# Performance work log

Hardware: AMD Instinct MI355X
Metric: run time of the kernel (lower is better)

The kernel has to match this reference:

```python
import jax, jax.numpy as jnp
import numpy as np

B, T, NE, NH, HD = 4, 1024, 768, 12, 64
CURV = 0.0
EPS = 1e-6
LN_EPS = 1e-5
ROPE_BASE = 10000.0


def project(x, k):
    # Lift Euclidean vector onto Lorentz hyperboloid with curvature K = exp(k):
    # time coord t = sqrt(K + ||x||^2) so that <lx, lx>_L = -K.
    K = jnp.exp(k)
    t = jnp.sqrt(K + jnp.sum(x * x, axis=-1, keepdims=True))
    return jnp.concatenate([t, x], axis=-1)


def lorentz_distance(lq, lk, k):
    # lq, lk: (B, H, T, D+1); k: (1, H, 1, 1) log-curvature.
    # d = sqrt(K) * arccosh(clamp(-<q,k>_L / K, 1+eps))
    K = jnp.exp(k)
    inner = (jnp.einsum('bhid,bhjd->bhij', lq[..., 1:], lk[..., 1:])
             - jnp.einsum('bhi,bhj->bhij', lq[..., 0], lk[..., 0]))
    c = jnp.clip(-inner / K, 1.0 + EPS, None)
    return jnp.sqrt(K) * jnp.arccosh(c)


def lorentz_norm(x):
    # sqrt(|<x,x>_L|) with <x,x>_L = -x0^2 + ||xs||^2  (keepdim)
    inner = -x[..., 0:1] ** 2 + jnp.sum(x[..., 1:] ** 2, axis=-1, keepdims=True)
    return jnp.sqrt(jnp.clip(-inner, EPS, None))


def rotary_tables():
    inv_freq = 1.0 / (ROPE_BASE ** (np.arange(0, HD, 2, dtype=np.float32) / HD))
    t = np.arange(T, dtype=np.float32)
    freqs = np.outer(t, inv_freq)  # (T, HD/2)
    cos = jnp.asarray(np.cos(freqs))[None, :, None, :]  # (1,T,1,HD/2)
    sin = jnp.asarray(np.sin(freqs))[None, :, None, :]
    return cos, sin


def apply_rotary(x, cos, sin):
    # x: (B, T, H, HD)
    x1, x2 = x[..., : HD // 2], x[..., HD // 2:]
    return jnp.concatenate([x1 * cos + x2 * sin, -x1 * sin + x2 * cos], axis=-1)


def layernorm(y, g, b):
    m = jnp.mean(y, axis=-1, keepdims=True)
    v = jnp.mean((y - m) ** 2, axis=-1, keepdims=True)
    return (y - m) / jnp.sqrt(v + LN_EPS) * g + b


def setup_inputs() -> dict:
    key = jax.random.key(0)
    ks = jax.random.split(key, 8)
    s = 0.02
    return {
        'x': jax.random.normal(ks[0], (B, T, NE), dtype=jnp.float32),
        'block_curvature': jnp.asarray(CURV, dtype=jnp.float32),
        'mlp_curvature': jnp.asarray(CURV, dtype=jnp.float32),
        'attn_curvatures': jnp.ones((1, NH, 1, 1), dtype=jnp.float32) * CURV,
        'qkv_w': jax.random.normal(ks[1], (3 * NE, NE + 1), dtype=jnp.float32) * s,
        'attn_proj_w': jax.random.normal(ks[2], (NE, (HD + 1) * NH), dtype=jnp.float32) * s,
        'attn_proj_b': jnp.zeros((NE,), dtype=jnp.float32),
        'mlp_expand_w': jax.random.normal(ks[3], (4 * NE + 3, NE + 1), dtype=jnp.float32) * s,
        'mlp_expand_b': jnp.zeros((4 * NE + 3,), dtype=jnp.float32),
        'mlp_shrink_w': jax.random.normal(ks[4], (NE, 4 * (NE + 1)), dtype=jnp.float32) * s,
        'mlp_shrink_b': jnp.zeros((NE,), dtype=jnp.float32),
        'ln_g': jnp.ones((NE,), dtype=jnp.float32),
        'ln_b': jnp.zeros((NE,), dtype=jnp.float32),
    }


def reference(x, block_curvature, mlp_curvature, attn_curvatures, qkv_w,
              attn_proj_w, attn_proj_b, mlp_expand_w, mlp_expand_b,
              mlp_shrink_w, mlp_shrink_b, ln_g, ln_b):
    cos, sin = rotary_tables()
    causal_bias = jnp.where(
        jnp.triu(jnp.ones((T, T), dtype=bool), k=1), -jnp.inf, 0.0).astype(jnp.float32)

    def block_norm(lx):
        return project(layernorm(lx[..., 1:], ln_g, ln_b), block_curvature)

    def attn(lx):
        qkv = lx @ qkv_w.T  # (B, T, 3*NE)
        q, k, v = jnp.split(qkv, 3, axis=-1)
        q = apply_rotary(q.reshape(B, T, NH, HD), cos, sin)
        k = apply_rotary(k.reshape(B, T, NH, HD), cos, sin)
        v = v.reshape(B, T, NH, HD)
        lq = project(q.transpose(0, 2, 1, 3), attn_curvatures)  # (B,H,T,HD+1)
        lk = project(k.transpose(0, 2, 1, 3), attn_curvatures)
        lv = project(v.transpose(0, 2, 1, 3), attn_curvatures)
        dis = lorentz_distance(lq, lk, attn_curvatures)  # (B,H,T,T)
        aw = jax.nn.softmax(-dis + causal_bias, axis=-1)
        a = jnp.einsum('bhij,bhjd->bhid', aw, lv)  # (B,H,T,HD+1)
        a = a * jnp.sqrt(jnp.exp(attn_curvatures)) / lorentz_norm(a)
        a = a.transpose(0, 2, 1, 3).reshape(B, T, NH * (HD + 1))
        a = a @ attn_proj_w.T + attn_proj_b
        return project(a, block_curvature)

    def mlp(lx):
        h = lx @ mlp_expand_w.T + mlp_expand_b  # (B,T,4*NE+3)
        h = project(h, mlp_curvature)[..., 1:]  # drop time coord back to 4*NE+3
        h = jax.nn.gelu(h, approximate=False)
        h = project(h, mlp_curvature)  # (B,T,4*(NE+1))
        h = h @ mlp_shrink_w.T + mlp_shrink_b
        return project(h, block_curvature)

    def skip(lx, f_lx):
        return project(lx[..., 1:] + f_lx[..., 1:], block_curvature)

    lx = project(x, block_curvature)  # (B,T,NE+1)
    lx = skip(lx, attn(block_norm(lx)))
    lx = skip(lx, mlp(block_norm(lx)))
    return lx
```

## Files before the change

kernel.cpp:

```cpp
#include <hip/hip_runtime.h>
#include <cmath>

typedef unsigned short ushort_t;
typedef __attribute__((ext_vector_type(8))) short short8;
typedef __attribute__((ext_vector_type(4))) float floatx4;

#define NH    12
#define T     1024
#define ROWS  4096
#define NE    768
#define KPA   832
#define KPB   3136
#define NEXP  3200
#define HEXP  3075
#define NSPLIT 3

__device__ __forceinline__ ushort_t f2bf(float f) {
  union { float f; unsigned u; } v; v.f = f;
  unsigned r = v.u + 0x7fffu + ((v.u >> 16) & 1u);
  return (ushort_t)(r >> 16);
}
__device__ __forceinline__ ushort_t f2bf_trunc(float f) {
  union { float f; unsigned u; } v; v.f = f;
  return (ushort_t)(v.u >> 16);
}
__device__ __forceinline__ float bf2f(ushort_t b) {
  union { unsigned u; float f; } v; v.u = ((unsigned)b) << 16;
  return v.f;
}
__device__ __forceinline__ float blk_reduce_sum(float v, float* sm) {
  #pragma unroll
  for (int o = 32; o > 0; o >>= 1) v += __shfl_xor(v, o, 64);
  int lane = threadIdx.x & 63, w = threadIdx.x >> 6;
  __syncthreads();
  if (lane == 0) sm[w] = v;
  __syncthreads();
  return sm[0] + sm[1] + sm[2] + sm[3];
}
__device__ __forceinline__ float red16_sum(float v) {
  #pragma unroll
  for (int o = 1; o < 16; o <<= 1) v += __shfl_xor(v, o, 64);
  return v;
}

#define NB_A 7488
#define NB_B 2496
#define NB_C 10400
#define NB_D 9408
#define NB_E 16
__device__ __forceinline__ void cvt_elem(ushort_t* __restrict__ dst,
                                         const float* __restrict__ src,
                                         int idx, int srcRows, int srcK, int dstK) {
  int r = idx / dstK, c = idx - r * dstK;
  dst[idx] = (r < srcRows && c < srcK) ? f2bf(src[(size_t)r * srcK + c]) : (ushort_t)0;
}
__global__ __launch_bounds__(256) void prep_kernel(
    ushort_t* __restrict__ qkv_wb, const float* __restrict__ qkvw,
    ushort_t* __restrict__ proj_wb, const float* __restrict__ projw,
    ushort_t* __restrict__ exp_wb, const float* __restrict__ expw,
    ushort_t* __restrict__ shr_wb, const float* __restrict__ shrw,
    ushort_t* __restrict__ aout_bf,
    const float* __restrict__ xin, const float* __restrict__ g,
    const float* __restrict__ bb, const float* __restrict__ curv,
    ushort_t* __restrict__ lnp) {
  __shared__ float sm[4];
  int blk = blockIdx.x;
  int tid = threadIdx.x;
  if (blk < NB_A) {
    cvt_elem(qkv_wb, qkvw, blk * 256 + tid, 2304, 769, KPA);
  } else if (blk < NB_A + NB_B) {
    cvt_elem(proj_wb, projw, (blk - NB_A) * 256 + tid, 768, 780, KPA);
  } else if (blk < NB_A + NB_B + NB_C) {
    cvt_elem(exp_wb, expw, (blk - NB_A - NB_B) * 256 + tid, HEXP, 769, KPA);
  } else if (blk < NB_A + NB_B + NB_C + NB_D) {
    cvt_elem(shr_wb, shrw, (blk - NB_A - NB_B - NB_C) * 256 + tid, 768, 3076, KPB);
  } else if (blk < NB_A + NB_B + NB_C + NB_D + NB_E) {
    int r = (blk - NB_A - NB_B - NB_C - NB_D) * 256 + tid;
    ushort_t* p = aout_bf + (size_t)r * KPA + 780;
    #pragma unroll
    for (int j = 0; j < KPA - 780; ++j) p[j] = 0;
  } else {
    const int row = blk - (NB_A + NB_B + NB_C + NB_D + NB_E);
    const float* xr = xin + (size_t)row * NE;
    float xv[3];
    float s = 0.f, ss = 0.f;
    #pragma unroll
    for (int i = 0; i < 3; ++i) {
      xv[i] = xr[tid + 256 * i];
      s += xv[i]; ss += xv[i] * xv[i];
    }
    s = blk_reduce_sum(s, sm);
    ss = blk_reduce_sum(ss, sm);
    float mean = s * (1.f / 768.f);
    float var = ss * (1.f / 768.f) - mean * mean;
    float rstd = rsqrtf(var + 1e-5f);
    float yv[3]; float ys = 0.f;
    #pragma unroll
    for (int i = 0; i < 3; ++i) {
      int c = tid + 256 * i;
      yv[i] = (xv[i] - mean) * rstd * g[c] + bb[c];
      ys += yv[i] * yv[i];
    }
    ys = blk_reduce_sum(ys, sm);
    float tc = sqrtf(expf(curv[0]) + ys);
    ushort_t* orow = lnp + (size_t)row * KPA;
    #pragma unroll
    for (int i = 0; i < 3; ++i) orow[1 + tid + 256 * i] = f2bf(yv[i]);
    if (tid == 0) orow[0] = f2bf(tc);
    if (tid < KPA - 769) orow[769 + tid] = 0;
  }
}

__global__ __launch_bounds__(256) void gemm_bf16(
    const ushort_t* __restrict__ A, int lda,
    const ushort_t* __restrict__ W, int ldw,
    void* __restrict__ Cout, int ldc,
    int nkTot, int cpt,
    const float* __restrict__ bias, int biasN,
    const float* __restrict__ res, int ldres,
    int outMode, void* __restrict__ Cp) {
  __shared__ ushort_t As[128 * 64];
  __shared__ ushort_t Bs[128 * 64];
  const int tid = threadIdx.x;
  const int w = tid >> 6, lane = tid & 63;
  const int rowBase = (int)blockIdx.y << 7;
  const int colBase = (int)blockIdx.x << 7;
  const int wm = (w & 1) * 64, wn = (w >> 1) * 64;
  const int lm = lane & 15, quad = lane >> 4;
  const int p0 = quad ^ (lm & 7);

  floatx4 acc[4][4];
  #pragma unroll
  for (int i = 0; i < 4; ++i)
    #pragma unroll
    for (int j = 0; j < 4; ++j) {
      floatx4 z = {0.f, 0.f, 0.f, 0.f};
      acc[i][j] = z;
    }

  const int kt0 = (int)blockIdx.z * cpt;
  const int kt1 = min(nkTot, kt0 + cpt);
  for (int kt = kt0; kt < kt1; ++kt) {
    __syncthreads();
    #pragma unroll
    for (int j = 0; j < 4; ++j) {
      int ci = j * 256 + tid;
      int r = ci >> 3;
      int g = (ci & 7) ^ (r & 7);
      const ushort_t* ga = A + (size_t)(rowBase + r) * lda + kt * 64 + g * 8;
      const ushort_t* gb = W + (size_t)(colBase + r) * ldw + kt * 64 + g * 8;
      __builtin_amdgcn_global_load_lds(
          (const __attribute__((address_space(1))) void*)ga,
          (__attribute__((address_space(3))) void*)&As[(j * 256 + w * 64) * 8],
          16, 0, 0);
      __builtin_amdgcn_global_load_lds(
          (const __attribute__((address_space(1))) void*)gb,
          (__attribute__((address_space(3))) void*)&Bs[(j * 256 + w * 64) * 8],
          16, 0, 0);
    }
    __syncthreads();

    #pragma unroll
    for (int s = 0; s < 2; ++s) {
      const int ps = s ? (p0 ^ 4) : p0;
      short8 af[4], bfr[4];
      #pragma unroll
      for (int i = 0; i < 4; ++i) {
        af[i]  = *(const short8*)&As[(wm + i * 16 + lm) * 64 + ps * 8];
        bfr[i] = *(const short8*)&Bs[(wn + i * 16 + lm) * 64 + ps * 8];
      }
      #pragma unroll
      for (int i = 0; i < 4; ++i)
        #pragma unroll
        for (int jn = 0; jn < 4; ++jn)
          acc[i][jn] = __builtin_amdgcn_mfma_f32_16x16x32_bf16(
              af[i], bfr[jn], acc[i][jn], 0, 0, 0);
    }
  }

  if (gridDim.z > 1) {
    ushort_t* dst = (ushort_t*)Cp + (size_t)blockIdx.z * ROWS * ldc;
    #pragma unroll
    for (int i = 0; i < 4; ++i)
      #pragma unroll
      for (int jn = 0; jn < 4; ++jn) {
        const int col = colBase + wn + jn * 16 + lm;
        #pragma unroll
        for (int rg = 0; rg < 4; ++rg) {
          const int row = rowBase + wm + i * 16 + quad * 4 + rg;
          dst[(size_t)row * ldc + col] = f2bf(acc[i][jn][rg]);
        }
      }
  } else if (outMode == 1) {
    ushort_t* C = (ushort_t*)Cout;
    #pragma unroll
    for (int i = 0; i < 4; ++i)
      #pragma unroll
      for (int jn = 0; jn < 4; ++jn) {
        const int col = colBase + wn + jn * 16 + lm;
        const float bv = bias ? ((col < biasN) ? bias[col] : 0.f) : 0.f;
        #pragma unroll
        for (int rg = 0; rg < 4; ++rg) {
          const int row = rowBase + wm + i * 16 + quad * 4 + rg;
          C[(size_t)row * ldc + col] = f2bf(acc[i][jn][rg] + bv);
        }
      }
  } else {
    float* C = (float*)Cout;
    #pragma unroll
    for (int i = 0; i < 4; ++i)
      #pragma unroll
      for (int jn = 0; jn < 4; ++jn) {
        const int col = colBase + wn + jn * 16 + lm;
        const float bv = bias ? ((col < biasN) ? bias[col] : 0.f) : 0.f;
        #pragma unroll
        for (int rg = 0; rg < 4; ++rg) {
          const int row = rowBase + wm + i * 16 + quad * 4 + rg;
          float o = acc[i][jn][rg] + bv;
          if (res) o += res[(size_t)row * ldres + col];
          C[(size_t)row * ldc + col] = o;
        }
      }
  }
}

__global__ __launch_bounds__(256) void rope_project(
    const ushort_t* __restrict__ qkv, const float* __restrict__ ac,
    ushort_t* __restrict__ qb, ushort_t* __restrict__ kb, ushort_t* __restrict__ vtb,
    float* __restrict__ q0, float* __restrict__ k0, float* __restrict__ v0) {
  int gid = blockIdx.x * 4 + (threadIdx.x >> 6);
  int lane = threadIdx.x & 63;
  int h = gid % NH;
  int bt = gid / NH;
  int t = bt & (T - 1);
  int b = bt >> 10;
  size_t base = (size_t)bt * 2304 + h * 64;
  float qv = bf2f(qkv[base + lane]);
  float kv = bf2f(qkv[base + 768 + lane]);
  float vv = bf2f(qkv[base + 1536 + lane]);
  int f = lane & 31;
  float ang = (float)t * powf(10000.f, -(float)f * (1.f / 32.f));
  float sn, cs;
  sincosf(ang, &sn, &cs);
  float qp = __shfl(qv, lane ^ 32, 64);
  float kp = __shfl(kv, lane ^ 32, 64);
  float qr = (lane < 32) ? (qv * cs + qp * sn) : (-qp * sn + qv * cs);
  float kr = (lane < 32) ? (kv * cs + kp * sn) : (-kp * sn + kv * cs);
  float Kh = expf(ac[h]);
  float sq = qr * qr, sk = kr * kr, sv = vv * vv;
  #pragma unroll
  for (int o = 32; o > 0; o >>= 1) {
    sq += __shfl_xor(sq, o, 64);
    sk += __shfl_xor(sk, o, 64);
    sv += __shfl_xor(sv, o, 64);
  }
  size_t idx = ((size_t)(b * NH + h) * T + t);
  qb[idx * 64 + lane] = f2bf(qr);
  kb[idx * 64 + lane] = f2bf(kr);
  vtb[(size_t)(b * NH + h) * (64 * T) + (size_t)lane * T + t] = f2bf(vv);
  if (lane == 0) {
    q0[idx] = sqrtf(Kh + sq);
    k0[idx] = sqrtf(Kh + sk);
    v0[idx] = sqrtf(Kh + sv);
  }
}

__global__ __launch_bounds__(256) void attn_kernel(
    const ushort_t* __restrict__ qb, const ushort_t* __restrict__ kb,
    const ushort_t* __restrict__ vtb,
    const float* __restrict__ q0, const float* __restrict__ k0,
    const float* __restrict__ v0,
    const float* __restrict__ ac,
    ushort_t* __restrict__ Opart, float* __restrict__ lpart,
    float* __restrict__ a0part) {
  __shared__ ushort_t Qs[64 * 64];
  __shared__ ushort_t Ks[64 * 64];
  __shared__ ushort_t Vts[64 * 64];
  __shared__ ushort_t Ps[64 * 72];

  const int sIdx = blockIdx.x;
  const int qtile = (int)gridDim.y - 1 - (int)blockIdx.y;
  const int bh = blockIdx.z;
  const int h = bh % NH;
  const int qt0 = qtile * 64;
  const int tid = threadIdx.x;
  const int w = tid >> 6, lane = tid & 63;
  const int lm = lane & 15, quad = lane >> 4;
  const int wm = w * 16;
  const int sw = lm & 7;

  const int n = qtile + 1;
  const int kbeg = (n * sIdx) / NSPLIT;
  const int kend = (n * (sIdx + 1)) / NSPLIT;
  const size_t pb = (size_t)(sIdx * 48 + bh) * T;

  if (kbeg >= kend) {
    #pragma unroll
    for (int r = 0; r < 4; ++r) {
      const int i = qt0 + wm + quad * 4 + r;
      ushort_t* orow = Opart + (pb + i) * 64;
      #pragma unroll
      for (int nt = 0; nt < 4; ++nt) orow[nt * 16 + lm] = 0;
      if (lm == 0) { lpart[pb + i] = 0.f; a0part[pb + i] = 0.f; }
    }
    return;
  }

  const float Kh = expf(ac[h]);
  const float sqrtK = sqrtf(Kh);
  const float invK = 1.0f / Kh;
  const float nsK = -sqrtK;
  const bool k1 = (Kh == 1.0f);

  {
    const ushort_t* qt = qb + ((size_t)bh * T + qt0) * 64;
    #pragma unroll
    for (int j = 0; j < 2; ++j) {
      int e = (j * 4 + w) * 512 + lane * 8;
      int r = e >> 6, chs = (e >> 3) & 7;
      int clog = (chs ^ (r & 7)) * 8;
      __builtin_amdgcn_global_load_lds(
          (const __attribute__((address_space(1))) void*)(qt + r * 64 + clog),
          (__attribute__((address_space(3))) void*)&Qs[(j * 4 + w) * 512],
          16, 0, 0);
    }
  }
  __syncthreads();
  short8 qf0 = *(const short8*)&Qs[(wm + lm) * 64 + ((0 + quad) ^ sw) * 8];
  short8 qf1 = *(const short8*)&Qs[(wm + lm) * 64 + ((4 + quad) ^ sw) * 8];
  float q0rv[4];
  #pragma unroll
  for (int r = 0; r < 4; ++r)
    q0rv[r] = q0[(size_t)bh * T + qt0 + wm + quad * 4 + r];

  float lsum[4], a0r[4];
  floatx4 oacc[4];
  #pragma unroll
  for (int r = 0; r < 4; ++r) { lsum[r] = 0.f; a0r[r] = 0.f; }
  #pragma unroll
  for (int nt = 0; nt < 4; ++nt) { floatx4 z = {0.f,0.f,0.f,0.f}; oacc[nt] = z; }

  for (int kt = kbeg; kt < kend; ++kt) {
    const int j0 = kt * 64;
    __syncthreads();
    {
      const ushort_t* ktile = kb + ((size_t)bh * T + j0) * 64;
      const ushort_t* vbh = vtb + (size_t)bh * (64 * T);
      #pragma unroll
      for (int j = 0; j < 2; ++j) {
        int e = (j * 4 + w) * 512 + lane * 8;
        int r = e >> 6, chs = (e >> 3) & 7;
        int clog = (chs ^ (r & 7)) * 8;
        __builtin_amdgcn_global_load_lds(
            (const __attribute__((address_space(1))) void*)(ktile + r * 64 + clog),
            (__attribute__((address_space(3))) void*)&Ks[(j * 4 + w) * 512],
            16, 0, 0);
        __builtin_amdgcn_global_load_lds(
            (const __attribute__((address_space(1))) void*)(vbh + (size_t)r * T + j0 + clog),
            (__attribute__((address_space(3))) void*)&Vts[(j * 4 + w) * 512],
            16, 0, 0);
      }
    }
    float k0i[4], v0v[4];
    #pragma unroll
    for (int jt = 0; jt < 4; ++jt) {
      k0i[jt] = k0[(size_t)bh * T + j0 + jt * 16 + lm] * invK;
      v0v[jt] = v0[(size_t)bh * T + j0 + jt * 16 + lm];
    }
    __syncthreads();

    floatx4 sacc[4];
    #pragma unroll
    for (int jt = 0; jt < 4; ++jt) {
      const int krow = jt * 16 + lm;
      short8 kf0 = *(const short8*)&Ks[krow * 64 + ((0 + quad) ^ sw) * 8];
      short8 kf1 = *(const short8*)&Ks[krow * 64 + ((4 + quad) ^ sw) * 8];
      floatx4 z = {0.f, 0.f, 0.f, 0.f};
      z = __builtin_amdgcn_mfma_f32_16x16x32_bf16(qf0, kf0, z, 0, 0, 0);
      z = __builtin_amdgcn_mfma_f32_16x16x32_bf16(qf1, kf1, z, 0, 0, 0);
      sacc[jt] = z;
    }

    const bool diag = (kt == qtile);
    if (k1) {
      #pragma unroll
      for (int r = 0; r < 4; ++r) {
        const int i = qt0 + wm + quad * 4 + r;
        float ls = 0.f, a0s = 0.f;
        #pragma unroll
        for (int jt = 0; jt < 4; ++jt) {
          float c = fmaf(-invK, sacc[jt][r], q0rv[r] * k0i[jt]);
          c = fmaxf(c, 1.000001f);
          float p = c - sqrtf(fmaf(c, c, -1.f));
          if (diag && (j0 + jt * 16 + lm > i)) p = 0.f;
          ushort_t pb2 = f2bf_trunc(p);
          Ps[(wm + quad * 4 + r) * 72 + jt * 16 + lm] = pb2;
          float pf = bf2f(pb2);
          ls += pf;
          a0s = fmaf(pf, v0v[jt], a0s);
        }
        lsum[r] += ls;
        a0r[r] += a0s;
      }
    } else {
      #pragma unroll
      for (int r = 0; r < 4; ++r) {
        const int i = qt0 + wm + quad * 4 + r;
        float ls = 0.f, a0s = 0.f;
        #pragma unroll
        for (int jt = 0; jt < 4; ++jt) {
          float c = fmaf(-invK, sacc[jt][r], q0rv[r] * k0i[jt]);
          c = fmaxf(c, 1.000001f);
          float z = c + sqrtf(fmaf(c, c, -1.f));
          float p = __builtin_amdgcn_exp2f(nsK * __builtin_amdgcn_logf(z));
          if (diag && (j0 + jt * 16 + lm > i)) p = 0.f;
          ushort_t pb2 = f2bf_trunc(p);
          Ps[(wm + quad * 4 + r) * 72 + jt * 16 + lm] = pb2;
          float pf = bf2f(pb2);
          ls += pf;
          a0s = fmaf(pf, v0v[jt], a0s);
        }
        lsum[r] += ls;
        a0r[r] += a0s;
      }
    }

    short8 pf0 = *(const short8*)&Ps[(wm + lm) * 72 + quad * 8];
    short8 pf1 = *(const short8*)&Ps[(wm + lm) * 72 + 32 + quad * 8];
    #pragma unroll
    for (int nt = 0; nt < 4; ++nt) {
      const int vrow = nt * 16 + lm;
      short8 vf0 = *(const short8*)&Vts[vrow * 64 + ((0 + quad) ^ sw) * 8];
      short8 vf1 = *(const short8*)&Vts[vrow * 64 + ((4 + quad) ^ sw) * 8];
      oacc[nt] = __builtin_amdgcn_mfma_f32_16x16x32_bf16(pf0, vf0, oacc[nt], 0, 0, 0);
      oacc[nt] = __builtin_amdgcn_mfma_f32_16x16x32_bf16(pf1, vf1, oacc[nt], 0, 0, 0);
    }
  }

  #pragma unroll
  for (int r = 0; r < 4; ++r) {
    float lf = red16_sum(lsum[r]);
    float a0f = red16_sum(a0r[r]);
    const int i = qt0 + wm + quad * 4 + r;
    ushort_t* orow = Opart + (pb + i) * 64;
    #pragma unroll
    for (int nt = 0; nt < 4; ++nt) orow[nt * 16 + lm] = f2bf(oacc[nt][r]);
    if (lm == 0) { lpart[pb + i] = lf; a0part[pb + i] = a0f; }
  }
}

__global__ __launch_bounds__(256) void attn_combine(
    const ushort_t* __restrict__ Opart, const float* __restrict__ lpart,
    const float* __restrict__ a0part,
    const float* __restrict__ ac, ushort_t* __restrict__ aout) {
  const int widx = blockIdx.x * 4 + (threadIdx.x >> 6);
  const int lane = threadIdx.x & 63;
  const int bh = widx >> 10;
  const int t = widx & 1023;
  const int h = bh % NH, b = bh / NH;
  float L = 0.f, A0 = 0.f, O = 0.f;
  #pragma unroll
  for (int sp = 0; sp < NSPLIT; ++sp) {
    const size_t r = (size_t)(sp * 48 + bh) * T + t;
    L += lpart[r];
    A0 += a0part[r];
    O += bf2f(Opart[r * 64 + lane]);
  }
  const float invl = 1.f / L;
  float av = O * invl;
  float ssq = av * av;
  #pragma unroll
  for (int o = 32; o > 0; o >>= 1) ssq += __shfl_xor(ssq, o, 64);
  float a0n = A0 * invl;
  float nsq = fmaxf(a0n * a0n - ssq, 1e-6f);
  float Kh = expf(ac[h]);
  float scale = sqrtf(Kh) * rsqrtf(nsq);
  ushort_t* orow = aout + (size_t)(b * T + t) * KPA + h * 65;
  orow[1 + lane] = f2bf(av * scale);
  if (lane == 0) orow[0] = f2bf(a0n * scale);
}

__global__ __launch_bounds__(256) void gelu_project(
    const ushort_t* __restrict__ hsrc, const float* __restrict__ curv,
    ushort_t* __restrict__ hp) {
  __shared__ float sm[4];
  const int row = blockIdx.x;
  const int tid = threadIdx.x;
  const ushort_t* hr = hsrc + (size_t)row * NEXP;
  float gv[13];
  float ss = 0.f;
  #pragma unroll
  for (int i = 0; i < 13; ++i) {
    int c = tid + 256 * i;
    float xx = (c < HEXP) ? bf2f(hr[c]) : 0.f;
    float gg = 0.5f * xx * (1.f + erff(xx * 0.70710678118654752f));
    gv[i] = gg; ss += gg * gg;
  }
  ss = blk_reduce_sum(ss, sm);
  float tc = sqrtf(expf(curv[0]) + ss);
  ushort_t* orow = hp + (size_t)row * KPB;
  #pragma unroll
  for (int i = 0; i < 13; ++i) {
    int c = tid + 256 * i;
    if (c < HEXP) orow[1 + c] = f2bf(gv[i]);
  }
  if (tid == 0) orow[0] = f2bf(tc);
  if (tid < KPB - (HEXP + 1)) orow[HEXP + 1 + tid] = 0;
}

__global__ __launch_bounds__(256) void reduce_ln_project(
    const ushort_t* __restrict__ Cp, int nsplit,
    const float* __restrict__ bias, const float* __restrict__ res,
    float* __restrict__ x2out,
    const float* __restrict__ g, const float* __restrict__ bb,
    const float* __restrict__ curv, ushort_t* __restrict__ lnp) {
  __shared__ float sm[4];
  const int row = blockIdx.x;
  const int tid = threadIdx.x;
  float xv[3];
  float s = 0.f, ss = 0.f;
  #pragma unroll
  for (int i = 0; i < 3; ++i) {
    const int c = tid + 256 * i;
    float v = bias[c] + res[(size_t)row * NE + c];
    for (int sp = 0; sp < nsplit; ++sp)
      v += bf2f(Cp[(size_t)sp * ROWS * NE + (size_t)row * NE + c]);
    x2out[(size_t)row * NE + c] = v;
    xv[i] = v;
    s += v; ss += v * v;
  }
  s = blk_reduce_sum(s, sm);
  ss = blk_reduce_sum(ss, sm);
  float mean = s * (1.f / 768.f);
  float var = ss * (1.f / 768.f) - mean * mean;
  float rstd = rsqrtf(var + 1e-5f);
  float yv[3]; float ys = 0.f;
  #pragma unroll
  for (int i = 0; i < 3; ++i) {
    int c = tid + 256 * i;
    yv[i] = (xv[i] - mean) * rstd * g[c] + bb[c];
    ys += yv[i] * yv[i];
  }
  ys = blk_reduce_sum(ys, sm);
  float tc = sqrtf(expf(curv[0]) + ys);
  ushort_t* orow = lnp + (size_t)row * KPA;
  #pragma unroll
  for (int i = 0; i < 3; ++i) orow[1 + tid + 256 * i] = f2bf(yv[i]);
  if (tid == 0) orow[0] = f2bf(tc);
  if (tid < KPA - 769) orow[769 + tid] = 0;
}

__global__ __launch_bounds__(256) void reduce_final_project(
    const ushort_t* __restrict__ Cp, int nsplit,
    const float* __restrict__ bias, const float* __restrict__ res,
    const float* __restrict__ curv, float* __restrict__ out) {
  __shared__ float sm[4];
  const int row = blockIdx.x;
  const int tid = threadIdx.x;
  float v[3]; float ss = 0.f;
  #pragma unroll
  for (int i = 0; i < 3; ++i) {
    const int c = tid + 256 * i;
    float t = bias[c] + res[(size_t)row * NE + c];
    for (int sp = 0; sp < nsplit; ++sp)
      t += bf2f(Cp[(size_t)sp * ROWS * NE + (size_t)row * NE + c]);
    v[i] = t; ss += t * t;
  }
  ss = blk_reduce_sum(ss, sm);
  float tc = sqrtf(expf(curv[0]) + ss);
  float* o = out + (size_t)row * 769;
  #pragma unroll
  for (int i = 0; i < 3; ++i) o[1 + tid + 256 * i] = v[i];
  if (tid == 0) o[0] = tc;
}

extern "C" void kernel_launch(void* const* d_in, const int* in_sizes, int n_in,
                              void* d_out, int out_size, void* d_ws, size_t ws_size,
                              hipStream_t stream) {
  (void)in_sizes; (void)n_in; (void)out_size; (void)ws_size;
  const float* x     = (const float*)d_in[0];
  const float* bc    = (const float*)d_in[1];
  const float* mc    = (const float*)d_in[2];
  const float* ac    = (const float*)d_in[3];
  const float* qkvw  = (const float*)d_in[4];
  const float* projw = (const float*)d_in[5];
  const float* projb = (const float*)d_in[6];
  const float* expw  = (const float*)d_in[7];
  const float* expb  = (const float*)d_in[8];
  const float* shrw  = (const float*)d_in[9];
  const float* shrb  = (const float*)d_in[10];
  const float* lng   = (const float*)d_in[11];
  const float* lnb   = (const float*)d_in[12];
  float* out = (float*)d_out;

  float* x2 = (float*)d_ws;
  ushort_t* qkv_wb  = (ushort_t*)(x2 + (size_t)ROWS * NE);
  ushort_t* proj_wb = qkv_wb + (size_t)2304 * KPA;
  ushort_t* exp_wb  = proj_wb + (size_t)768 * KPA;
  ushort_t* shr_wb  = exp_wb + (size_t)NEXP * KPA;
  ushort_t* lnp_bf  = shr_wb + (size_t)768 * KPB;
  ushort_t* aout_bf = lnp_bf + (size_t)ROWS * KPA;
  char* r2 = (char*)(aout_bf + (size_t)ROWS * KPA);
  ushort_t* qkvb = (ushort_t*)r2;
  ushort_t* qbb = qkvb + (size_t)ROWS * 2304;
  ushort_t* kbb = qbb + (size_t)48 * T * 64;
  ushort_t* vtb = kbb + (size_t)48 * T * 64;
  float* q0b = (float*)(vtb + (size_t)48 * T * 64);
  float* k0b = q0b + (size_t)48 * T;
  float* v0b = k0b + (size_t)48 * T;
  ushort_t* Opart = (ushort_t*)(v0b + (size_t)48 * T);
  float* lpart = (float*)(Opart + (size_t)NSPLIT * 48 * T * 64);
  float* a0part = lpart + (size_t)NSPLIT * 48 * T;
  ushort_t* ppartP = (ushort_t*)r2;
  ushort_t* hbbf = (ushort_t*)r2;
  ushort_t* hp_bf = hbbf + (size_t)ROWS * NEXP;
  ushort_t* ppartS = hp_bf + (size_t)ROWS * KPB;

  prep_kernel<<<NB_A + NB_B + NB_C + NB_D + NB_E + ROWS, 256, 0, stream>>>(
      qkv_wb, qkvw, proj_wb, projw, exp_wb, expw, shr_wb, shrw, aout_bf,
      x, lng, lnb, bc, lnp_bf);
  gemm_bf16<<<dim3(2304 / 128, ROWS / 128, 1), 256, 0, stream>>>(
      lnp_bf, KPA, qkv_wb, KPA, qkvb, 2304, KPA / 64, KPA / 64,
      nullptr, 0, nullptr, 0, 1, nullptr);
  rope_project<<<(ROWS * NH) / 4, 256, 0, stream>>>(qkvb, ac, qbb, kbb, vtb, q0b, k0b, v0b);
  attn_kernel<<<dim3(NSPLIT, T / 64, 48), 256, 0, stream>>>(
      qbb, kbb, vtb, q0b, k0b, v0b, ac, Opart, lpart, a0part);
  attn_combine<<<(48 * T) / 4, 256, 0, stream>>>(Opart, lpart, a0part, ac, aout_bf);
  gemm_bf16<<<dim3(768 / 128, ROWS / 128, 2), 256, 0, stream>>>(
      aout_bf, KPA, proj_wb, KPA, nullptr, NE, KPA / 64, 7,
      nullptr, 0, nullptr, 0, 0, ppartP);
  reduce_ln_project<<<ROWS, 256, 0, stream>>>(
      ppartP, 2, projb, x, x2, lng, lnb, bc, lnp_bf);
  gemm_bf16<<<dim3(NEXP / 128, ROWS / 128, 1), 256, 0, stream>>>(
      lnp_bf, KPA, exp_wb, KPA, hbbf, NEXP, KPA / 64, KPA / 64,
      expb, HEXP, nullptr, 0, 1, nullptr);
  gelu_project<<<ROWS, 256, 0, stream>>>(hbbf, mc, hp_bf);
  gemm_bf16<<<dim3(768 / 128, ROWS / 128, 4), 256, 0, stream>>>(
      hp_bf, KPB, shr_wb, KPB, nullptr, NE, KPB / 64, 13,
      nullptr, 0, nullptr, 0, 0, ppartS);
  reduce_final_project<<<ROWS, 256, 0, stream>>>(
      ppartS, 4, shrb, x2, bc, out);
}
```

Measured before the change: 376.2 us.

## Double-buffer GEMM and attention tile loads; widen attention query tile to 128

The bf16 GEMM now double-buffers its A and B shared-memory tiles. It issues the next k-tile's global-to-LDS loads before running the MFMAs on the current tile, which cuts the per-iteration barrier count to one. The attention kernel moves to 512-thread blocks covering 128 query rows, with double-buffered K/V tiles and the k0/v0 row scalars prefetched one tile ahead. Rope's powf is replaced with a hardware exp2 using a precomputed log2 constant. In exchange, LDS use per block is higher and the attention grid has fewer, larger blocks, which may lower occupancy and worsen load balance across the causal split.

```diff
diff --git a/kernel.cpp b/kernel.cpp
--- a/kernel.cpp
+++ b/kernel.cpp
@@ -119,8 +119,8 @@
     const float* __restrict__ bias, int biasN,
     const float* __restrict__ res, int ldres,
     int outMode, void* __restrict__ Cp) {
-  __shared__ ushort_t As[128 * 64];
-  __shared__ ushort_t Bs[128 * 64];
+  __shared__ ushort_t As[2][128 * 64];
+  __shared__ ushort_t Bs[2][128 * 64];
   const int tid = threadIdx.x;
   const int w = tid >> 6, lane = tid & 63;
   const int rowBase = (int)blockIdx.y << 7;
@@ -140,8 +140,8 @@
 
   const int kt0 = (int)blockIdx.z * cpt;
   const int kt1 = min(nkTot, kt0 + cpt);
-  for (int kt = kt0; kt < kt1; ++kt) {
-    __syncthreads();
+
+  auto stage = [&](int kt, int bsel) {
     #pragma unroll
     for (int j = 0; j < 4; ++j) {
       int ci = j * 256 + tid;
@@ -151,14 +151,24 @@
       const ushort_t* gb = W + (size_t)(colBase + r) * ldw + kt * 64 + g * 8;
       __builtin_amdgcn_global_load_lds(
           (const __attribute__((address_space(1))) void*)ga,
-          (__attribute__((address_space(3))) void*)&As[(j * 256 + w * 64) * 8],
+          (__attribute__((address_space(3))) void*)&As[bsel][(j * 256 + w * 64) * 8],
           16, 0, 0);
       __builtin_amdgcn_global_load_lds(
           (const __attribute__((address_space(1))) void*)gb,
-          (__attribute__((address_space(3))) void*)&Bs[(j * 256 + w * 64) * 8],
+          (__attribute__((address_space(3))) void*)&Bs[bsel][(j * 256 + w * 64) * 8],
           16, 0, 0);
     }
-    __syncthreads();
+  };
+
+  stage(kt0, 0);
+  asm volatile("s_waitcnt vmcnt(0)" ::: "memory");
+  __builtin_amdgcn_s_barrier();
+  __builtin_amdgcn_sched_barrier(0);
+
+  int cur = 0;
+  for (int kt = kt0; kt < kt1; ++kt) {
+    const bool hasNext = (kt + 1 < kt1);
+    if (hasNext) stage(kt + 1, cur ^ 1);
 
     #pragma unroll
     for (int s = 0; s < 2; ++s) {
@@ -166,8 +176,8 @@
       short8 af[4], bfr[4];
       #pragma unroll
       for (int i = 0; i < 4; ++i) {
-        af[i]  = *(const short8*)&As[(wm + i * 16 + lm) * 64 + ps * 8];
-        bfr[i] = *(const short8*)&Bs[(wn + i * 16 + lm) * 64 + ps * 8];
+        af[i]  = *(const short8*)&As[cur][(wm + i * 16 + lm) * 64 + ps * 8];
+        bfr[i] = *(const short8*)&Bs[cur][(wn + i * 16 + lm) * 64 + ps * 8];
       }
       #pragma unroll
       for (int i = 0; i < 4; ++i)
@@ -176,6 +186,13 @@
           acc[i][jn] = __builtin_amdgcn_mfma_f32_16x16x32_bf16(
               af[i], bfr[jn], acc[i][jn], 0, 0, 0);
     }
+
+    if (hasNext) {
+      asm volatile("s_waitcnt vmcnt(0)" ::: "memory");
+      __builtin_amdgcn_s_barrier();
+      __builtin_amdgcn_sched_barrier(0);
+    }
+    cur ^= 1;
   }
 
   if (gridDim.z > 1) {
@@ -239,7 +256,7 @@
   float kv = bf2f(qkv[base + 768 + lane]);
   float vv = bf2f(qkv[base + 1536 + lane]);
   int f = lane & 31;
-  float ang = (float)t * powf(10000.f, -(float)f * (1.f / 32.f));
+  float ang = (float)t * __builtin_amdgcn_exp2f(-(float)f * 0.4152410118661534f);
   float sn, cs;
   sincosf(ang, &sn, &cs);
   float qp = __shfl(qv, lane ^ 32, 64);
@@ -265,7 +282,7 @@
   }
 }
 
-__global__ __launch_bounds__(256) void attn_kernel(
+__global__ __launch_bounds__(512, 4) void attn_kernel(
     const ushort_t* __restrict__ qb, const ushort_t* __restrict__ kb,
     const ushort_t* __restrict__ vtb,
     const float* __restrict__ q0, const float* __restrict__ k0,
@@ -273,23 +290,23 @@
     const float* __restrict__ ac,
     ushort_t* __restrict__ Opart, float* __restrict__ lpart,
     float* __restrict__ a0part) {
-  __shared__ ushort_t Qs[64 * 64];
-  __shared__ ushort_t Ks[64 * 64];
-  __shared__ ushort_t Vts[64 * 64];
-  __shared__ ushort_t Ps[64 * 72];
+  __shared__ ushort_t Qs[128 * 64];
+  __shared__ ushort_t Ks[2][64 * 64];
+  __shared__ ushort_t Vts[2][64 * 64];
+  __shared__ ushort_t Ps[128 * 72];
 
   const int sIdx = blockIdx.x;
   const int qtile = (int)gridDim.y - 1 - (int)blockIdx.y;
   const int bh = blockIdx.z;
   const int h = bh % NH;
-  const int qt0 = qtile * 64;
+  const int qt0 = qtile * 128;
   const int tid = threadIdx.x;
   const int w = tid >> 6, lane = tid & 63;
   const int lm = lane & 15, quad = lane >> 4;
   const int wm = w * 16;
   const int sw = lm & 7;
 
-  const int n = qtile + 1;
+  const int n = 2 * qtile + 2;
   const int kbeg = (n * sIdx) / NSPLIT;
   const int kend = (n * (sIdx + 1)) / NSPLIT;
   const size_t pb = (size_t)(sIdx * 48 + bh) * T;
@@ -313,26 +330,51 @@
   const bool k1 = (Kh == 1.0f);
 
   {
-    const ushort_t* qt = qb + ((size_t)bh * T + qt0) * 64;
+    const ushort_t* qtp = qb + ((size_t)bh * T + qt0) * 64;
     #pragma unroll
     for (int j = 0; j < 2; ++j) {
-      int e = (j * 4 + w) * 512 + lane * 8;
-      int r = e >> 6, chs = (e >> 3) & 7;
-      int clog = (chs ^ (r & 7)) * 8;
+      int ci = j * 512 + tid;
+      int r = ci >> 3;
+      int clog = ((ci & 7) ^ (r & 7)) * 8;
       __builtin_amdgcn_global_load_lds(
-          (const __attribute__((address_space(1))) void*)(qt + r * 64 + clog),
-          (__attribute__((address_space(3))) void*)&Qs[(j * 4 + w) * 512],
+          (const __attribute__((address_space(1))) void*)(qtp + r * 64 + clog),
+          (__attribute__((address_space(3))) void*)&Qs[(j * 8 + w) * 512],
           16, 0, 0);
     }
   }
-  __syncthreads();
-  short8 qf0 = *(const short8*)&Qs[(wm + lm) * 64 + ((0 + quad) ^ sw) * 8];
-  short8 qf1 = *(const short8*)&Qs[(wm + lm) * 64 + ((4 + quad) ^ sw) * 8];
+  const ushort_t* kbase = kb + (size_t)bh * T * 64;
+  const ushort_t* vbh = vtb + (size_t)bh * (64 * T);
+  const float* k0row = k0 + (size_t)bh * T;
+  const float* v0row = v0 + (size_t)bh * T;
+  const int ldr = tid >> 3;
+  const int ldcs = ((tid & 7) ^ (ldr & 7)) * 8;
+  {
+    const int j0 = kbeg * 64;
+    __builtin_amdgcn_global_load_lds(
+        (const __attribute__((address_space(1))) void*)(kbase + (size_t)(j0 + ldr) * 64 + ldcs),
+        (__attribute__((address_space(3))) void*)&Ks[0][w * 512], 16, 0, 0);
+    __builtin_amdgcn_global_load_lds(
+        (const __attribute__((address_space(1))) void*)(vbh + (size_t)ldr * T + j0 + ldcs),
+        (__attribute__((address_space(3))) void*)&Vts[0][w * 512], 16, 0, 0);
+  }
+  float k0n[4], v0n[4];
+  #pragma unroll
+  for (int jt = 0; jt < 4; ++jt) {
+    k0n[jt] = k0row[kbeg * 64 + jt * 16 + lm];
+    v0n[jt] = v0row[kbeg * 64 + jt * 16 + lm];
+  }
   float q0rv[4];
   #pragma unroll
   for (int r = 0; r < 4; ++r)
     q0rv[r] = q0[(size_t)bh * T + qt0 + wm + quad * 4 + r];
 
+  asm volatile("s_waitcnt vmcnt(0)" ::: "memory");
+  __builtin_amdgcn_s_barrier();
+  __builtin_amdgcn_sched_barrier(0);
+
+  const short8 qf0 = *(const short8*)&Qs[(wm + lm) * 64 + ((0 + quad) ^ sw) * 8];
+  const short8 qf1 = *(const short8*)&Qs[(wm + lm) * 64 + ((4 + quad) ^ sw) * 8];
+
   float lsum[4], a0r[4];
   floatx4 oacc[4];
   #pragma unroll
@@ -340,48 +382,45 @@
   #pragma unroll
   for (int nt = 0; nt < 4; ++nt) { floatx4 z = {0.f,0.f,0.f,0.f}; oacc[nt] = z; }
 
+  int cur = 0;
   for (int kt = kbeg; kt < kend; ++kt) {
+    const bool hasNext = (kt + 1 < kend);
+    float k0i[4], v0v[4];
+    #pragma unroll
+    for (int jt = 0; jt < 4; ++jt) { k0i[jt] = k0n[jt] * invK; v0v[jt] = v0n[jt]; }
+
+    if (hasNext) {
+      const int j0n = (kt + 1) * 64;
+      __builtin_amdgcn_global_load_lds(
+          (const __attribute__((address_space(1))) void*)(kbase + (size_t)(j0n + ldr) * 64 + ldcs),
+          (__attribute__((address_space(3))) void*)&Ks[cur ^ 1][w * 512], 16, 0, 0);
+      __builtin_amdgcn_global_load_lds(
+          (const __attribute__((address_space(1))) void*)(vbh + (size_t)ldr * T + j0n + ldcs),
+          (__attribute__((address_space(3))) void*)&Vts[cur ^ 1][w * 512], 16, 0, 0);
+      #pragma unroll
+      for (int jt = 0; jt < 4; ++jt) {
+        k0n[jt] = k0row[j0n + jt * 16 + lm];
+        v0n[jt] = v0row[j0n + jt * 16 + lm];
+      }
+    }
+
     const int j0 = kt * 64;
-    __syncthreads();
-    {
-      const ushort_t* ktile = kb + ((size_t)bh * T + j0) * 64;
-      const ushort_t* vbh = vtb + (size_t)bh * (64 * T);
-      #pragma unroll
-      for (int j = 0; j < 2; ++j) {
-        int e = (j * 4 + w) * 512 + lane * 8;
-        int r = e >> 6, chs = (e >> 3) & 7;
-        int clog = (chs ^ (r & 7)) * 8;
-        __builtin_amdgcn_global_load_lds(
-            (const __attribute__((address_space(1))) void*)(ktile + r * 64 + clog),
-            (__attribute__((address_space(3))) void*)&Ks[(j * 4 + w) * 512],
-            16, 0, 0);
-        __builtin_amdgcn_global_load_lds(
-            (const __attribute__((address_space(1))) void*)(vbh + (size_t)r * T + j0 + clog),
-            (__attribute__((address_space(3))) void*)&Vts[(j * 4 + w) * 512],
-            16, 0, 0);
-      }
-    }
-    float k0i[4], v0v[4];
-    #pragma unroll
-    for (int jt = 0; jt < 4; ++jt) {
-      k0i[jt] = k0[(size_t)bh * T + j0 + jt * 16 + lm] * invK;
-      v0v[jt] = v0[(size_t)bh * T + j0 + jt * 16 + lm];
-    }
-    __syncthreads();
+    const ushort_t* Kc = Ks[cur];
+    const ushort_t* Vc = Vts[cur];
 
     floatx4 sacc[4];
     #pragma unroll
     for (int jt = 0; jt < 4; ++jt) {
       const int krow = jt * 16 + lm;
-      short8 kf0 = *(const short8*)&Ks[krow * 64 + ((0 + quad) ^ sw) * 8];
-      short8 kf1 = *(const short8*)&Ks[krow * 64 + ((4 + quad) ^ sw) * 8];
+      short8 kf0 = *(const short8*)&Kc[krow * 64 + ((0 + quad) ^ sw) * 8];
+      short8 kf1 = *(const short8*)&Kc[krow * 64 + ((4 + quad) ^ sw) * 8];
       floatx4 z = {0.f, 0.f, 0.f, 0.f};
       z = __builtin_amdgcn_mfma_f32_16x16x32_bf16(qf0, kf0, z, 0, 0, 0);
       z = __builtin_amdgcn_mfma_f32_16x16x32_bf16(qf1, kf1, z, 0, 0, 0);
       sacc[jt] = z;
     }
 
-    const bool diag = (kt == qtile);
+    const bool maskT = (kt >= 2 * qtile);
     if (k1) {
       #pragma unroll
       for (int r = 0; r < 4; ++r) {
@@ -392,7 +431,7 @@
           float c = fmaf(-invK, sacc[jt][r], q0rv[r] * k0i[jt]);
           c = fmaxf(c, 1.000001f);
           float p = c - sqrtf(fmaf(c, c, -1.f));
-          if (diag && (j0 + jt * 16 + lm > i)) p = 0.f;
+          if (maskT && (j0 + jt * 16 + lm > i)) p = 0.f;
           ushort_t pb2 = f2bf_trunc(p);
           Ps[(wm + quad * 4 + r) * 72 + jt * 16 + lm] = pb2;
           float pf = bf2f(pb2);
@@ -413,7 +452,7 @@
           c = fmaxf(c, 1.000001f);
           float z = c + sqrtf(fmaf(c, c, -1.f));
           float p = __builtin_amdgcn_exp2f(nsK * __builtin_amdgcn_logf(z));
-          if (diag && (j0 + jt * 16 + lm > i)) p = 0.f;
+          if (maskT && (j0 + jt * 16 + lm > i)) p = 0.f;
           ushort_t pb2 = f2bf_trunc(p);
           Ps[(wm + quad * 4 + r) * 72 + jt * 16 + lm] = pb2;
           float pf = bf2f(pb2);
@@ -430,11 +469,18 @@
     #pragma unroll
     for (int nt = 0; nt < 4; ++nt) {
       const int vrow = nt * 16 + lm;
-      short8 vf0 = *(const short8*)&Vts[vrow * 64 + ((0 + quad) ^ sw) * 8];
-      short8 vf1 = *(const short8*)&Vts[vrow * 64 + ((4 + quad) ^ sw) * 8];
+      short8 vf0 = *(const short8*)&Vc[vrow * 64 + ((0 + quad) ^ sw) * 8];
+      short8 vf1 = *(const short8*)&Vc[vrow * 64 + ((4 + quad) ^ sw) * 8];
       oacc[nt] = __builtin_amdgcn_mfma_f32_16x16x32_bf16(pf0, vf0, oacc[nt], 0, 0, 0);
       oacc[nt] = __builtin_amdgcn_mfma_f32_16x16x32_bf16(pf1, vf1, oacc[nt], 0, 0, 0);
     }
+
+    if (hasNext) {
+      asm volatile("s_waitcnt vmcnt(0)" ::: "memory");
+      __builtin_amdgcn_s_barrier();
+      __builtin_amdgcn_sched_barrier(0);
+    }
+    cur ^= 1;
   }
 
   #pragma unroll
@@ -623,7 +669,7 @@
       lnp_bf, KPA, qkv_wb, KPA, qkvb, 2304, KPA / 64, KPA / 64,
       nullptr, 0, nullptr, 0, 1, nullptr);
   rope_project<<<(ROWS * NH) / 4, 256, 0, stream>>>(qkvb, ac, qbb, kbb, vtb, q0b, k0b, v0b);
-  attn_kernel<<<dim3(NSPLIT, T / 64, 48), 256, 0, stream>>>(
+  attn_kernel<<<dim3(NSPLIT, T / 128, 48), 512, 0, stream>>>(
       qbb, kbb, vtb, q0b, k0b, v0b, ac, Opart, lpart, a0part);
   attn_combine<<<(48 * T) / 4, 256, 0, stream>>>(Opart, lpart, a0part, ac, aout_bf);
   gemm_bf16<<<dim3(768 / 128, ROWS / 128, 2), 256, 0, stream>>>(
```

Measured after the change: 381.5 us. About the same (+1.4%).
